# Performance work log

Measured on AMD Instinct MI355X. Metric: run time of the kernel, lower is better.

The kernel has to match this reference:

```python
import jax, jax.numpy as jnp
import numpy as np

TAU = 2.0
DECAY = float(np.exp(-1.0 / TAU))
THRESH = 1.0  # base_threshold; adaptive update only happens in training mode
LN_EPS = 1e-5
B, S, V, D, L = 16, 256, 32000, 512, 4  # d_state must equal d_model (see shape_source)

@jax.custom_vjp
def atan_spike(x):
    # spikingjelly surrogate.ATan: heaviside fwd, atan surrogate bwd (alpha=2)
    return (x >= 0).astype(x.dtype)

def _atan_fwd(x):
    return atan_spike(x), x

def _atan_bwd(x, g):
    alpha = 2.0
    s = (jnp.pi / 2.0) * alpha * x
    return (g * (alpha / 2.0) / (1.0 + s * s),)

atan_spike.defvjp(_atan_fwd, _atan_bwd)

def lif_step(mem, x):
    mem = mem * DECAY + x
    spike = atan_spike(mem - THRESH)
    mem = mem * (1.0 - jax.lax.stop_gradient(spike))  # reset uses spike.detach()
    return mem, spike

def layer_norm(x, g, b):
    m = jnp.mean(x, axis=-1, keepdims=True)
    v = jnp.mean(jnp.square(x - m), axis=-1, keepdims=True)
    return (x - m) / jnp.sqrt(v + LN_EPS) * g + b

def setup_inputs():
    key = jax.random.key(0)
    ks = jax.random.split(key, 8)
    s = 0.02
    return {
        'input_ids': jax.random.randint(ks[0], (B, S), 0, V),
        'embedding': jax.random.normal(ks[1], (V, D), jnp.float32) * s,
        'enc_W': jax.random.normal(ks[2], (D, D), jnp.float32) * s,
        'enc_b': jnp.zeros((D,), jnp.float32),
        'gen_W': jax.random.normal(ks[3], (L, D, D), jnp.float32) * s,
        'gen_b': jnp.zeros((L, D), jnp.float32),
        'inf_W': jax.random.normal(ks[4], (L, D, D), jnp.float32) * s,
        'inf_b': jnp.zeros((L, D), jnp.float32),
        'err_g': jnp.ones((L, D), jnp.float32),
        'err_b': jnp.zeros((L, D), jnp.float32),
        'st_g': jnp.ones((L, D), jnp.float32),
        'st_b': jnp.zeros((L, D), jnp.float32),
        'out_W': jax.random.normal(ks[5], (V, D), jnp.float32) * s,
        'out_b': jnp.zeros((V,), jnp.float32),
    }

def reference(input_ids, embedding, enc_W, enc_b, gen_W, gen_b, inf_W, inf_b, err_g, err_b, st_g, st_b, out_W, out_b):
    tok = embedding[input_ids]              # [B,S,D]
    xs = jnp.swapaxes(tok, 0, 1)            # [S,B,D] scan over time

    def pc_layer(j, gm, im, bottom_up, top_down):
        # PredictiveCodingLayer.forward (LIF mems gm/im are persistent state)
        gm, pred = lif_step(gm, top_down @ gen_W[j].T + gen_b[j])
        err = layer_norm(jax.nn.relu(bottom_up - pred), err_g[j], err_b[j])
        im, su = lif_step(im, err @ inf_W[j].T + inf_b[j])
        new_state = layer_norm(top_down + su, st_g[j], st_b[j])
        return gm, im, new_state, err, pred

    def step(carry, emb_t):
        enc_mem, gen_mem, inf_mem, states, spk, memp = carry
        enc_mem, bu = lif_step(enc_mem, emb_t @ enc_W.T + enc_b)
        # bottom-up pass
        for j in range(L):
            gm, im, st, err, _ = pc_layer(j, gen_mem[j], inf_mem[j], bu, states[j])
            gen_mem = gen_mem.at[j].set(gm)
            inf_mem = inf_mem.at[j].set(im)
            states = states.at[j].set(st)
            bu = jax.nn.relu(st)
            spk = spk + err.mean()
            memp = memp + jnp.abs(im).mean()
        # top-down generative pass (same layers called again: mems keep evolving)
        td = states[L - 1]
        zb = jnp.zeros_like(bu)
        for j in reversed(range(L)):
            gm, im, _, _, pred = pc_layer(j, gen_mem[j], inf_mem[j], zb, td)
            gen_mem = gen_mem.at[j].set(gm)
            inf_mem = inf_mem.at[j].set(im)
            td = pred
        logits = td @ out_W.T + out_b
        return (enc_mem, gen_mem, inf_mem, states, spk, memp), logits

    init = (jnp.zeros((B, D), jnp.float32), jnp.zeros((L, B, D), jnp.float32),
            jnp.zeros((L, B, D), jnp.float32), jnp.zeros((L, B, D), jnp.float32),
            jnp.float32(0.0), jnp.float32(0.0))
    (_, _, _, _, spk, memp), logits_sb = jax.lax.scan(step, init, xs)
    final_logits = jnp.swapaxes(logits_sb, 0, 1)  # [B,S,V]
    return final_logits, spk / S, memp / S
```

## Files before the change

### kernel.cpp

```cpp
#include <hip/hip_runtime.h>
#include <math.h>

#define S_ 256
#define B_ 16
#define D_ 512
#define V_ 32000
#define L_ 4
#define DEC_ 0.6065306597126334f

typedef short v8s __attribute__((ext_vector_type(8)));
typedef float v4f __attribute__((ext_vector_type(4)));

static __device__ __forceinline__ short f2bf(float f){
  union { float f; unsigned u; } v; v.f = f;
  unsigned r = (v.u + 0x7FFFu + ((v.u >> 16) & 1u)) >> 16;
  return (short)(unsigned short)r;
}

__global__ __launch_bounds__(256) void k_gemm_enc(const int* __restrict__ ids,
                                                  const float* __restrict__ emb,
                                                  const float* __restrict__ encW,
                                                  const float* __restrict__ encb,
                                                  float* __restrict__ X,
                                                  unsigned* __restrict__ counts,
                                                  unsigned* __restrict__ bunz,
                                                  float* __restrict__ accum){
  __shared__ __align__(16) short As[64*40];
  __shared__ __align__(16) short Bs[64*40];
  __shared__ int ids_s[64];
  const int t = threadIdx.x;
  const int bm = blockIdx.x, bn = blockIdx.y;
  if (bn == 0 && bm < 16){
    int g = bm*256 + t;
    counts[g] = 0u;
    bunz[g] = 0u;
    if (g < 2) accum[g] = 0.0f;
  }
  if (t < 64){
    int mg = bm*64 + t;
    int s = mg >> 4, b = mg & 15;
    ids_s[t] = ids[b * S_ + s];
  }
  __syncthreads();
  const int arow = t >> 2;
  const int kc = (t & 3) * 8;
  const int wave = t >> 6;
  const int l = t & 63;
  const int lm = l & 15;
  const int q = l >> 4;
  v4f acc[4] = {};
  for (int k0 = 0; k0 < D_; k0 += 32){
    const float* asrc = emb + (size_t)ids_s[arow] * D_ + k0 + kc;
    float4 a0 = *(const float4*)asrc;
    float4 a1 = *(const float4*)(asrc + 4);
    const float* bsrc = encW + (size_t)(bn*64 + arow) * D_ + k0 + kc;
    float4 b0 = *(const float4*)bsrc;
    float4 b1 = *(const float4*)(bsrc + 4);
    v8s av, bv;
    av[0]=f2bf(a0.x); av[1]=f2bf(a0.y); av[2]=f2bf(a0.z); av[3]=f2bf(a0.w);
    av[4]=f2bf(a1.x); av[5]=f2bf(a1.y); av[6]=f2bf(a1.z); av[7]=f2bf(a1.w);
    bv[0]=f2bf(b0.x); bv[1]=f2bf(b0.y); bv[2]=f2bf(b0.z); bv[3]=f2bf(b0.w);
    bv[4]=f2bf(b1.x); bv[5]=f2bf(b1.y); bv[6]=f2bf(b1.z); bv[7]=f2bf(b1.w);
    *(v8s*)&As[arow*40 + kc] = av;
    *(v8s*)&Bs[arow*40 + kc] = bv;
    __syncthreads();
    v8s af = *(const v8s*)&As[(wave*16 + lm)*40 + q*8];
    #pragma unroll
    for (int n = 0; n < 4; ++n){
      v8s bf = *(const v8s*)&Bs[(n*16 + lm)*40 + q*8];
      acc[n] = __builtin_amdgcn_mfma_f32_16x16x32_bf16(af, bf, acc[n], 0, 0, 0);
    }
    __syncthreads();
  }
  #pragma unroll
  for (int n = 0; n < 4; ++n){
    #pragma unroll
    for (int i = 0; i < 4; ++i){
      int mloc = wave*16 + q*4 + i;
      int nloc = n*16 + lm;
      int r  = bm*64 + mloc;
      int nn = bn*64 + nloc;
      X[(size_t)r * D_ + nn] = acc[n][i] + encb[nn];
    }
  }
}

__global__ __launch_bounds__(64) void k_scan(const float* __restrict__ X,
                                             unsigned char* __restrict__ bu,
                                             unsigned* __restrict__ bunz,
                                             const float* __restrict__ inf_W,
                                             const float* __restrict__ inf_b,
                                             const float* __restrict__ err_b,
                                             float* __restrict__ cvec){
  int bx = blockIdx.x;
  if (bx >= 128){
    int r = bx - 128;
    int j = r >> 3;
    int dp = (r & 7) * 64 + threadIdx.x;
    const float* row = inf_W + ((size_t)j * D_ + dp) * D_;
    const float* eb = err_b + j * D_;
    float acc = inf_b[j * D_ + dp];
    for (int d = 0; d < D_; d += 8){
      float4 w0 = *(const float4*)(row + d);
      float4 w1 = *(const float4*)(row + d + 4);
      float4 e0 = *(const float4*)(eb + d);
      float4 e1 = *(const float4*)(eb + d + 4);
      acc += e0.x*w0.x + e0.y*w0.y + e0.z*w0.z + e0.w*w0.w;
      acc += e1.x*w1.x + e1.y*w1.y + e1.z*w1.z + e1.w*w1.w;
    }
    cvec[j * D_ + dp] = acc;
    return;
  }
  int g = bx * 64 + threadIdx.x;
  int b = g >> 9;
  float mem = 0.0f;
  for (int s0 = 0; s0 < S_; s0 += 8){
    float x[8];
    #pragma unroll
    for (int i = 0; i < 8; ++i) x[i] = X[(size_t)(s0 + i) * (B_*D_) + g];
    #pragma unroll
    for (int i = 0; i < 8; ++i){
      mem = mem * DEC_ + x[i];
      float sp = (mem >= 1.0f) ? 1.0f : 0.0f;
      mem *= (1.0f - sp);
      bu[(size_t)(s0 + i) * (B_*D_) + g] = (unsigned char)sp;
      if (sp != 0.0f) atomicOr(&bunz[(s0 + i) * B_ + b], 1u);
    }
  }
}

__device__ __forceinline__ float wave_sum(float x){
  #pragma unroll
  for (int o = 32; o > 0; o >>= 1) x += __shfl_xor(x, o);
  return x;
}

__device__ void wave_matvec(const float* __restrict__ W, const float* __restrict__ bias,
                            const float x[8], float y[8], float* xs, int l){
  __syncthreads();
  #pragma unroll
  for (int i = 0; i < 8; ++i) xs[l + 64*i] = x[i];
  __syncthreads();
  #pragma unroll
  for (int i = 0; i < 8; ++i){
    int dp = l + 64*i;
    const float* row = W + (size_t)dp * D_;
    float acc = bias[dp];
    for (int d = 0; d < D_; d += 4){
      float4 w = *(const float4*)(row + d);
      acc += xs[d]*w.x + xs[d+1]*w.y + xs[d+2]*w.z + xs[d+3]*w.w;
    }
    y[i] = acc;
  }
}

__device__ void wave_ln(const float e[8], const float* __restrict__ g,
                        const float* __restrict__ bb, float out[8], int l){
  float s = 0.f;
  #pragma unroll
  for (int i = 0; i < 8; ++i) s += e[i];
  float m = wave_sum(s) * (1.0f/512.0f);
  float s2 = 0.f;
  #pragma unroll
  for (int i = 0; i < 8; ++i){ float d = e[i] - m; s2 += d*d; }
  float var = wave_sum(s2) * (1.0f/512.0f);
  float inv = 1.0f / sqrtf(var + 1e-5f);
  #pragma unroll
  for (int i = 0; i < 8; ++i){
    int d = l + 64*i;
    out[i] = (e[i] - m) * inv * g[d] + bb[d];
  }
}

__global__ __launch_bounds__(64) void k_sim(
    const float* __restrict__ gen_W, const float* __restrict__ gen_b,
    const float* __restrict__ inf_W, const float* __restrict__ inf_b,
    const float* __restrict__ err_g, const float* __restrict__ err_b,
    const float* __restrict__ st_g, const float* __restrict__ st_b,
    const unsigned char* __restrict__ bu8, const unsigned* __restrict__ bunz,
    const float* __restrict__ cvec,
    unsigned* __restrict__ counts, unsigned short* __restrict__ idxb,
    float* __restrict__ accum)
{
  const int b = blockIdx.x, l = threadIdx.x;
  __shared__ float xs[D_];
  __shared__ unsigned scnt;
  float st[4][8], gm[4][8], im[4][8];
  #pragma unroll
  for (int j = 0; j < 4; ++j)
    #pragma unroll
    for (int i = 0; i < 8; ++i){ st[j][i]=0.f; gm[j][i]=0.f; im[j][i]=0.f; }

  bool okz = true;
  #pragma unroll
  for (int j = 0; j < 4; ++j)
    #pragma unroll
    for (int i = 0; i < 8; ++i){
      int d = j*512 + l + 64*i;
      okz = okz && (gen_b[d]==0.f) && (inf_b[d]==0.f) && (err_b[d]==0.f) && (st_b[d]==0.f);
    }
  const bool bias_zero = (__all((int)okz) != 0);

  unsigned long long fl[4];
  #pragma unroll
  for (int w = 0; w < 4; ++w){
    unsigned v = bunz[(w*64 + l) * B_ + b];
    fl[w] = __ballot(v != 0u);
  }

  bool state_zero = true;
  float spk_acc = 0.f, memp_acc = 0.f;

  for (int t = 0; t < S_; ++t){
    bool nz = ((fl[t >> 6] >> (t & 63)) & 1ull) != 0ull;
    if (state_zero && bias_zero && !nz) continue;
    state_zero = false;

    float bu[8];
    #pragma unroll
    for (int i = 0; i < 8; ++i) bu[i] = (float)bu8[(size_t)(t*B_ + b)*D_ + l + 64*i];

    #pragma unroll
    for (int j = 0; j < 4; ++j){
      float y[8];
      wave_matvec(gen_W + (size_t)j*D_*D_, gen_b + j*D_, st[j], y, xs, l);
      float pred[8];
      #pragma unroll
      for (int i = 0; i < 8; ++i){
        gm[j][i] = gm[j][i]*DEC_ + y[i];
        pred[i] = (gm[j][i] >= 1.0f) ? 1.0f : 0.0f;
        gm[j][i] *= (1.0f - pred[i]);
      }
      float e[8];
      #pragma unroll
      for (int i = 0; i < 8; ++i){ float v = bu[i] - pred[i]; e[i] = v > 0.f ? v : 0.f; }
      float eo[8];
      wave_ln(e, err_g + j*D_, err_b + j*D_, eo, l);
      #pragma unroll
      for (int i = 0; i < 8; ++i) spk_acc += eo[i];
      float y2[8];
      wave_matvec(inf_W + (size_t)j*D_*D_, inf_b + j*D_, eo, y2, xs, l);
      float su[8];
      #pragma unroll
      for (int i = 0; i < 8; ++i){
        im[j][i] = im[j][i]*DEC_ + y2[i];
        su[i] = (im[j][i] >= 1.0f) ? 1.0f : 0.0f;
        im[j][i] *= (1.0f - su[i]);
        memp_acc += fabsf(im[j][i]);
      }
      float tmp[8];
      #pragma unroll
      for (int i = 0; i < 8; ++i) tmp[i] = st[j][i] + su[i];
      wave_ln(tmp, st_g + j*D_, st_b + j*D_, st[j], l);
      #pragma unroll
      for (int i = 0; i < 8; ++i) bu[i] = st[j][i] > 0.f ? st[j][i] : 0.f;
    }

    float td[8];
    #pragma unroll
    for (int i = 0; i < 8; ++i) td[i] = st[3][i];
    #pragma unroll
    for (int j = 3; j >= 0; --j){
      float y[8];
      wave_matvec(gen_W + (size_t)j*D_*D_, gen_b + j*D_, td, y, xs, l);
      #pragma unroll
      for (int i = 0; i < 8; ++i){
        gm[j][i] = gm[j][i]*DEC_ + y[i];
        float p = (gm[j][i] >= 1.0f) ? 1.0f : 0.0f;
        gm[j][i] *= (1.0f - p);
        td[i] = p;
      }
      #pragma unroll
      for (int i = 0; i < 8; ++i){
        float c = cvec[j*D_ + l + 64*i];
        im[j][i] = im[j][i]*DEC_ + c;
        float ss = (im[j][i] >= 1.0f) ? 1.0f : 0.0f;
        im[j][i] *= (1.0f - ss);
      }
    }

    if (l == 0) scnt = 0u;
    __syncthreads();
    unsigned base = (unsigned)(t*B_ + b) * D_;
    #pragma unroll
    for (int i = 0; i < 8; ++i){
      if (td[i] != 0.f){
        unsigned pos = atomicAdd(&scnt, 1u);
        idxb[base + pos] = (unsigned short)(l + 64*i);
      }
    }
    __syncthreads();
    if (l == 0) counts[t*B_ + b] = scnt;
  }
  spk_acc = wave_sum(spk_acc);
  memp_acc = wave_sum(memp_acc);
  if (l == 0){
    atomicAdd(&accum[0], spk_acc);
    atomicAdd(&accum[1], memp_acc);
  }
}

__global__ __launch_bounds__(64) void k_logits(const unsigned* __restrict__ counts,
                                               const unsigned short* __restrict__ idxb,
                                               const float* __restrict__ outW,
                                               const float* __restrict__ outb,
                                               const float* __restrict__ accum,
                                               float* __restrict__ out){
  const int chunk = blockIdx.x % 25;
  const int rg = blockIdx.x / 25;
  const int lane = threadIdx.x;
  if (blockIdx.x == 0 && lane == 0){
    const float inv = 1.0f / (float)(B_ * D_ * S_);
    out[(size_t)B_ * S_ * V_ + 0] = accum[0] * inv;
    out[(size_t)B_ * S_ * V_ + 1] = accum[1] * inv;
  }
  const int colbase = chunk * 1280;
  v4f pay[5];
  #pragma unroll
  for (int k = 0; k < 5; ++k)
    pay[k] = *(const v4f*)(outb + colbase + k*256 + lane*4);

  int prow = rg*32 + (lane & 31);
  unsigned myc = counts[(prow & 255) * B_ + (prow >> 8)];

  for (int r = 0; r < 32; ++r){
    int row = rg*32 + r;
    unsigned cnt = (unsigned)__shfl((int)myc, r);
    float* dst = out + (size_t)row * V_ + colbase;
    if (cnt == 0){
      #pragma unroll
      for (int k = 0; k < 5; ++k)
        __builtin_nontemporal_store(pay[k], (v4f*)(dst + k*256 + lane*4));
    } else {
      int s = row & 255, b = row >> 8;
      unsigned base = (unsigned)(s * B_ + b) * D_;
      v4f acc[5];
      #pragma unroll
      for (int k = 0; k < 5; ++k) acc[k] = pay[k];
      for (unsigned i = 0; i < cnt; ++i){
        int d = idxb[base + i];
        #pragma unroll
        for (int k = 0; k < 5; ++k){
          int v = colbase + k*256 + lane*4;
          acc[k].x += outW[(size_t)(v+0)*D_ + d];
          acc[k].y += outW[(size_t)(v+1)*D_ + d];
          acc[k].z += outW[(size_t)(v+2)*D_ + d];
          acc[k].w += outW[(size_t)(v+3)*D_ + d];
        }
      }
      #pragma unroll
      for (int k = 0; k < 5; ++k)
        __builtin_nontemporal_store(acc[k], (v4f*)(dst + k*256 + lane*4));
    }
  }
}

extern "C" void kernel_launch(void* const* d_in, const int* in_sizes, int n_in,
                              void* d_out, int out_size, void* d_ws, size_t ws_size,
                              hipStream_t stream){
  (void)in_sizes; (void)n_in; (void)out_size; (void)ws_size;
  const int*   input_ids = (const int*)d_in[0];
  const float* embedding = (const float*)d_in[1];
  const float* enc_W = (const float*)d_in[2];
  const float* enc_b = (const float*)d_in[3];
  const float* gen_W = (const float*)d_in[4];
  const float* gen_b = (const float*)d_in[5];
  const float* inf_W = (const float*)d_in[6];
  const float* inf_b = (const float*)d_in[7];
  const float* err_g = (const float*)d_in[8];
  const float* err_b = (const float*)d_in[9];
  const float* st_g  = (const float*)d_in[10];
  const float* st_b  = (const float*)d_in[11];
  const float* out_W = (const float*)d_in[12];
  const float* out_b = (const float*)d_in[13];
  float* out = (float*)d_out;
  char* ws = (char*)d_ws;

  float*          X      = (float*)(ws + 0);
  unsigned char*  bu     = (unsigned char*)(ws + 8388608);
  unsigned short* idxb   = (unsigned short*)(ws + 10485760);
  unsigned*       counts = (unsigned*)(ws + 14680064);
  unsigned*       bunz   = (unsigned*)(ws + 14696448);
  float*          cvec   = (float*)(ws + 14712832);
  float*          accum  = (float*)(ws + 14721024);

  hipLaunchKernelGGL(k_gemm_enc, dim3(64, 8), dim3(256), 0, stream,
                     input_ids, embedding, enc_W, enc_b, X, counts, bunz, accum);
  hipLaunchKernelGGL(k_scan, dim3(160), dim3(64), 0, stream,
                     X, bu, bunz, inf_W, inf_b, err_b, cvec);
  hipLaunchKernelGGL(k_sim, dim3(16), dim3(64), 0, stream,
                     gen_W, gen_b, inf_W, inf_b, err_g, err_b, st_g, st_b,
                     bu, bunz, cvec, counts, idxb, accum);
  hipLaunchKernelGGL(k_logits, dim3(3200), dim3(64), 0, stream,
                     counts, idxb, out_W, out_b, accum, out);
}
```

Before: 705.0 us.

## Overlap bias-fill of logits with serial sim kernel, then sparse-fix spiking rows

The sequential simulation kernel uses only 16 blocks, so extra blocks are added to the same launch to write out_b into the whole logits buffer while the simulation runs. A small follow-up kernel then revisits only the rows with nonzero spikes and adds the selected out_W columns in place. This hides the large logits write behind the latency-bound scan. In exchange, rows with spikes are read back and rewritten, and the fix kernel is serialized across only 128 blocks. The extra blocks may also contend with the simulation blocks for memory bandwidth.

```diff
diff --git a/kernel.cpp b/kernel.cpp
--- a/kernel.cpp
+++ b/kernel.cpp
@@ -172,7 +172,7 @@
   }
 }
 
-__global__ __launch_bounds__(64) void k_sim(
+__global__ __launch_bounds__(64) void k_simstream(
     const float* __restrict__ gen_W, const float* __restrict__ gen_b,
     const float* __restrict__ inf_W, const float* __restrict__ inf_b,
     const float* __restrict__ err_g, const float* __restrict__ err_b,
@@ -180,11 +180,32 @@
     const unsigned char* __restrict__ bu8, const unsigned* __restrict__ bunz,
     const float* __restrict__ cvec,
     unsigned* __restrict__ counts, unsigned short* __restrict__ idxb,
-    float* __restrict__ accum)
+    float* __restrict__ accum,
+    const float* __restrict__ outb, float* __restrict__ out)
 {
-  const int b = blockIdx.x, l = threadIdx.x;
   __shared__ float xs[D_];
   __shared__ unsigned scnt;
+
+  if (blockIdx.x >= 16){
+    const int sbx = blockIdx.x - 16;
+    const int chunk = sbx % 25;
+    const int rg = sbx / 25;
+    const int lane = threadIdx.x;
+    const int colbase = chunk * 1280;
+    v4f pay[5];
+    #pragma unroll
+    for (int k = 0; k < 5; ++k)
+      pay[k] = *(const v4f*)(outb + colbase + k*256 + lane*4);
+    for (int r = 0; r < 32; ++r){
+      float* dst = out + (size_t)(rg*32 + r) * V_ + colbase;
+      #pragma unroll
+      for (int k = 0; k < 5; ++k)
+        *(v4f*)(dst + k*256 + lane*4) = pay[k];
+    }
+    return;
+  }
+
+  const int b = blockIdx.x, l = threadIdx.x;
   float st[4][8], gm[4][8], im[4][8];
   #pragma unroll
   for (int j = 0; j < 4; ++j)
@@ -300,57 +321,39 @@
   }
 }
 
-__global__ __launch_bounds__(64) void k_logits(const unsigned* __restrict__ counts,
-                                               const unsigned short* __restrict__ idxb,
-                                               const float* __restrict__ outW,
-                                               const float* __restrict__ outb,
-                                               const float* __restrict__ accum,
-                                               float* __restrict__ out){
-  const int chunk = blockIdx.x % 25;
-  const int rg = blockIdx.x / 25;
+__global__ __launch_bounds__(64) void k_fix(const unsigned* __restrict__ counts,
+                                            const unsigned short* __restrict__ idxb,
+                                            const float* __restrict__ outW,
+                                            const float* __restrict__ accum,
+                                            float* __restrict__ out){
   const int lane = threadIdx.x;
-  if (blockIdx.x == 0 && lane == 0){
+  const int rg = blockIdx.x;
+  if (rg == 0 && lane == 0){
     const float inv = 1.0f / (float)(B_ * D_ * S_);
     out[(size_t)B_ * S_ * V_ + 0] = accum[0] * inv;
     out[(size_t)B_ * S_ * V_ + 1] = accum[1] * inv;
   }
-  const int colbase = chunk * 1280;
-  v4f pay[5];
-  #pragma unroll
-  for (int k = 0; k < 5; ++k)
-    pay[k] = *(const v4f*)(outb + colbase + k*256 + lane*4);
-
   int prow = rg*32 + (lane & 31);
   unsigned myc = counts[(prow & 255) * B_ + (prow >> 8)];
-
+  if (__ballot(myc != 0u) == 0ull) return;
   for (int r = 0; r < 32; ++r){
+    unsigned cnt = (unsigned)__shfl((int)myc, r);
+    if (cnt == 0u) continue;
     int row = rg*32 + r;
-    unsigned cnt = (unsigned)__shfl((int)myc, r);
-    float* dst = out + (size_t)row * V_ + colbase;
-    if (cnt == 0){
-      #pragma unroll
-      for (int k = 0; k < 5; ++k)
-        __builtin_nontemporal_store(pay[k], (v4f*)(dst + k*256 + lane*4));
-    } else {
-      int s = row & 255, b = row >> 8;
-      unsigned base = (unsigned)(s * B_ + b) * D_;
-      v4f acc[5];
-      #pragma unroll
-      for (int k = 0; k < 5; ++k) acc[k] = pay[k];
+    int s = row & 255, b = row >> 8;
+    unsigned base = (unsigned)(s * B_ + b) * D_;
+    float* dst = out + (size_t)row * V_;
+    for (int c = 0; c < 125; ++c){
+      int off = c*256 + lane*4;
+      v4f a = *(v4f*)(dst + off);
       for (unsigned i = 0; i < cnt; ++i){
         int d = idxb[base + i];
-        #pragma unroll
-        for (int k = 0; k < 5; ++k){
-          int v = colbase + k*256 + lane*4;
-          acc[k].x += outW[(size_t)(v+0)*D_ + d];
-          acc[k].y += outW[(size_t)(v+1)*D_ + d];
-          acc[k].z += outW[(size_t)(v+2)*D_ + d];
-          acc[k].w += outW[(size_t)(v+3)*D_ + d];
-        }
-      }
-      #pragma unroll
-      for (int k = 0; k < 5; ++k)
-        __builtin_nontemporal_store(acc[k], (v4f*)(dst + k*256 + lane*4));
+        a.x += outW[(size_t)(off+0)*D_ + d];
+        a.y += outW[(size_t)(off+1)*D_ + d];
+        a.z += outW[(size_t)(off+2)*D_ + d];
+        a.w += outW[(size_t)(off+3)*D_ + d];
+      }
+      *(v4f*)(dst + off) = a;
     }
   }
 }
@@ -388,9 +391,9 @@
                      input_ids, embedding, enc_W, enc_b, X, counts, bunz, accum);
   hipLaunchKernelGGL(k_scan, dim3(160), dim3(64), 0, stream,
                      X, bu, bunz, inf_W, inf_b, err_b, cvec);
-  hipLaunchKernelGGL(k_sim, dim3(16), dim3(64), 0, stream,
+  hipLaunchKernelGGL(k_simstream, dim3(16 + 3200), dim3(64), 0, stream,
                      gen_W, gen_b, inf_W, inf_b, err_g, err_b, st_g, st_b,
-                     bu, bunz, cvec, counts, idxb, accum);
-  hipLaunchKernelGGL(k_logits, dim3(3200), dim3(64), 0, stream,
-                     counts, idxb, out_W, out_b, accum, out);
-}
+                     bu, bunz, cvec, counts, idxb, accum, out_b, out);
+  hipLaunchKernelGGL(k_fix, dim3(128), dim3(64), 0, stream,
+                     counts, idxb, out_W, accum, out);
+}
```

New measurement: 683.7 us (median of 2 runs). 3.0% less time.
